# Kernel optimization log

Hardware: AMD Instinct MI355X
Metric: run time of the kernel (lower is better)

The kernel has to match this reference:

```python
import jax, jax.numpy as jnp
import numpy as np

KH, KW = 3, 3
STRIDE, PAD, DIL = 1, 1, 1
DG = 1  # deformable groups


def setup_inputs() -> dict:
    key = jax.random.key(0)
    k1, k2, k3, k4 = jax.random.split(key, 4)
    B, C, H, W, O = 4, 64, 128, 128, 64
    x = jax.random.normal(k1, (B, C, H, W), jnp.float32)
    weight = jax.random.normal(k2, (O, C, KH, KW), jnp.float32) * 0.05
    bias = jnp.zeros((O,), jnp.float32)
    # offset/mask conv params (zero-init in original; small random here so
    # the bilinear sampling path is actually exercised)
    om_weight = jax.random.normal(k3, (DG * 3 * KH * KW, C, KH, KW), jnp.float32) * 0.01
    om_bias = jax.random.normal(k4, (DG * 3 * KH * KW,), jnp.float32) * 0.01
    return {"x": x, "weight": weight, "bias": bias,
            "om_weight": om_weight, "om_bias": om_bias}


def _dcn(x, weight, bias, om_weight, om_bias):
    B, C, H, W = x.shape
    O = weight.shape[0]
    K = KH * KW
    Cg = C // DG

    # --- offset/mask conv (plain conv2d) ---
    om = jax.lax.conv_general_dilated(
        x, om_weight, (STRIDE, STRIDE), [(PAD, PAD), (PAD, PAD)],
        dimension_numbers=("NCHW", "OIHW", "NCHW"))
    om = om + om_bias[None, :, None, None]
    Ho, Wo = om.shape[2], om.shape[3]
    o1, o2, m = jnp.split(om, 3, axis=1)            # each (B, DG*K, Ho, Wo)
    off_y = o1.reshape(B, DG, K, Ho, Wo)
    off_x = o2.reshape(B, DG, K, Ho, Wo)
    mask = jax.nn.sigmoid(m).reshape(B, DG, K, Ho, Wo)

    # --- fractional sampling positions per kernel tap ---
    ky = jnp.repeat(jnp.arange(KH), KW).astype(jnp.float32)   # (K,)
    kx = jnp.tile(jnp.arange(KW), KH).astype(jnp.float32)
    base_y = (jnp.arange(Ho, dtype=jnp.float32) * STRIDE - PAD)
    base_x = (jnp.arange(Wo, dtype=jnp.float32) * STRIDE - PAD)
    py = off_y + base_y[None, None, None, :, None] + (ky * DIL)[None, None, :, None, None]
    px = off_x + base_x[None, None, None, None, :] + (kx * DIL)[None, None, :, None, None]

    y0 = jnp.floor(py)
    x0 = jnp.floor(px)
    ly = py - y0
    lx = px - x0
    y0i = y0.astype(jnp.int32)
    x0i = x0.astype(jnp.int32)

    xg = x.reshape(B, DG, Cg, H * W)
    # gather spatial samples per (batch, group), broadcast over channels
    gather = jax.vmap(jax.vmap(lambda feat, idx: jnp.take(feat, idx, axis=-1)))

    def corner(yc, xc, w):
        valid = (yc >= 0) & (yc < H) & (xc >= 0) & (xc < W)
        idx = jnp.clip(yc, 0, H - 1) * W + jnp.clip(xc, 0, W - 1)  # (B,DG,K,Ho,Wo)
        v = gather(xg, idx.reshape(B, DG, -1)).reshape(B, DG, Cg, K, Ho, Wo)
        w = jnp.where(valid, w, 0.0)
        return v * w[:, :, None]  # zero-padded bilinear corner

    val = (corner(y0i,     x0i,     (1 - ly) * (1 - lx))
         + corner(y0i,     x0i + 1, (1 - ly) * lx)
         + corner(y0i + 1, x0i,     ly * (1 - lx))
         + corner(y0i + 1, x0i + 1, ly * lx))
    val = val * mask[:, :, None]                    # (B,DG,Cg,K,Ho,Wo)

    w4 = weight.reshape(O, DG, Cg, K)
    out = jnp.einsum("ogck,bgckhw->bohw", w4, val) + bias[None, :, None, None]
    return out


def reference(x, weight, bias, om_weight, om_bias):
    return _dcn(x, weight, bias, om_weight, om_bias)
```

## Files before the change

kernel.cpp:

```cpp
#include <hip/hip_runtime.h>
#include <hip/hip_fp16.h>
#include <math.h>

#define BB 4
#define CC 64
#define HH 128
#define WW 128
#define OO 64
#define HWW (HH * WW)

typedef _Float16 f16x8 __attribute__((ext_vector_type(8)));
typedef float f32x4 __attribute__((ext_vector_type(4)));

#define WHF_OFF  0
#define WLF_OFF  73728
#define WOMH_OFF 147456
#define WOML_OFF 184320

__device__ inline __half2 u2h(unsigned u) {
    union { unsigned u; __half2 h; } c; c.u = u; return c.h;
}
__device__ inline unsigned h2u(__half2 h) {
    union { __half2 h; unsigned u; } c; c.h = h; return c.u;
}

__global__ void prep_kernel(const float* __restrict__ weight,
                            const float* __restrict__ om_weight,
                            unsigned short* __restrict__ whf,
                            unsigned short* __restrict__ wlf,
                            unsigned short* __restrict__ womh,
                            unsigned short* __restrict__ woml)
{
    int d = blockIdx.x * 256 + threadIdx.x;
    if (d < 18 * 4 * 64 * 8) {
        int j  = d & 7;
        int l  = (d >> 3) & 63;
        int wv = (d >> 9) & 3;
        int ch = d >> 11;
        int o  = wv * 16 + (l & 15);
        int kk = (l >> 4) * 8 + j;
        int c  = (ch / 9) * 32 + kk;
        int tap = ch % 9;
        float w = weight[(o * CC + c) * 9 + tap];
        __half h = __float2half_rn(w);
        __half lo = __float2half_rn(w - __half2float(h));
        whf[d] = __half_as_ushort(h);
        wlf[d] = __half_as_ushort(lo);
    }
    int d2 = d - 18 * 4 * 64 * 8;
    if (d2 >= 0 && d2 < 18 * 2 * 64 * 8) {
        int j  = d2 & 7;
        int l  = (d2 >> 3) & 63;
        int og = (d2 >> 9) & 1;
        int ch = d2 >> 10;
        int o  = og * 16 + (l & 15);
        int kk = (l >> 4) * 8 + j;
        int c  = (ch / 9) * 32 + kk;
        int tap = ch % 9;
        float w = (o < 27) ? om_weight[(o * CC + c) * 9 + tap] : 0.f;
        __half h = __float2half_rn(w);
        __half lo = __float2half_rn(w - __half2float(h));
        womh[d2] = __half_as_ushort(h);
        woml[d2] = __half_as_ushort(lo);
    }
}

__global__ void __launch_bounds__(256, 4)
fused_kernel(const float* __restrict__ x,
             const unsigned short* __restrict__ whf,
             const unsigned short* __restrict__ wlf,
             const unsigned short* __restrict__ womh,
             const unsigned short* __restrict__ woml,
             const float* __restrict__ bias,
             const float* __restrict__ om_bias,
             float* __restrict__ out)
{
    __shared__ __align__(16) uint4 Xw[8 * 180];
    __shared__ __align__(16) uint4 vex[2][32][9];
    __shared__ __align__(16) uint4 swth4[288];
    __shared__ int sidx[288];

    int t    = threadIdx.x;
    int lane = t & 63;
    int wv   = t >> 6;

    int bid = blockIdx.x;
    int b   = bid >> 9;
    int r   = bid & 511;
    int ho  = r >> 2;
    int w0  = (r & 3) << 5;

    {
        const float* xb = x + (size_t)b * CC * HWW;
#pragma unroll 1
        for (int i = t; i < 8 * 180; i += 256) {
            int cg  = i / 180;
            int pos = i - cg * 180;
            int rr  = pos / 36;
            int cc2 = pos - rr * 36;
            int gy = ho - 2 + rr, gx = w0 - 2 + cc2;
            bool ok = (gy >= 0) & (gy < HH) & (gx >= 0) & (gx < WW);
            int gi = ok ? gy * WW + gx : 0;
            const float* xc = xb + (size_t)cg * 8 * HWW + gi;
            float v0 = xc[0],       v1 = xc[HWW],     v2 = xc[2 * HWW], v3 = xc[3 * HWW];
            float v4 = xc[4 * HWW], v5 = xc[5 * HWW], v6 = xc[6 * HWW], v7 = xc[7 * HWW];
            if (!ok) { v0=0.f; v1=0.f; v2=0.f; v3=0.f; v4=0.f; v5=0.f; v6=0.f; v7=0.f; }
            uint4 p;
            p.x = h2u(__floats2half2_rn(v0, v1));
            p.y = h2u(__floats2half2_rn(v2, v3));
            p.z = h2u(__floats2half2_rn(v4, v5));
            p.w = h2u(__floats2half2_rn(v6, v7));
            Xw[cg * 180 + pos] = p;
        }
    }
    __syncthreads();

    f32x4 accom = (f32x4){0.f, 0.f, 0.f, 0.f};
    {
        int og = wv & 1;
        int s  = wv >> 1;
        int pix_s = s * 16 + (lane & 15);
        int oct   = lane >> 4;
#pragma unroll 1
        for (int ch = 0; ch < 18; ch++) {
            int half = ch / 9;
            int tap  = ch - half * 9;
            int ky = tap / 3, kx = tap - ky * 3;
            int pos = (ky + 1) * 36 + pix_s + kx + 1;
            uint4 pw = Xw[(half * 4 + oct) * 180 + pos];
            union { f16x8 v; uint4 u; } B; B.u = pw;
            const f16x8 ah = *(const f16x8*)&womh[((size_t)(ch * 2 + og) * 64 + lane) * 8];
            const f16x8 al = *(const f16x8*)&woml[((size_t)(ch * 2 + og) * 64 + lane) * 8];
            accom = __builtin_amdgcn_mfma_f32_16x16x32_f16(ah, B.v, accom, 0, 0, 0);
            accom = __builtin_amdgcn_mfma_f32_16x16x32_f16(al, B.v, accom, 0, 0, 0);
        }
    }

    float* omL = (float*)&vex[0][0][0];
    {
        int og = wv & 1, s = wv >> 1;
#pragma unroll
        for (int rg = 0; rg < 4; rg++) {
            int m = og * 16 + (lane >> 4) * 4 + rg;
            if (m < 27) {
                int pp = s * 16 + (lane & 15);
                float v = accom[rg] + om_bias[m];
                if (m >= 18) v = 1.f / (1.f + expf(-v));
                omL[m * 32 + pp] = v;
            }
        }
    }
    __syncthreads();

#pragma unroll 1
    for (int it = t; it < 288; it += 256) {
        int k  = it >> 5;
        int pp = it & 31;
        float oy = omL[k * 32 + pp];
        float ox = omL[(9 + k) * 32 + pp];
        float mm = omL[(18 + k) * 32 + pp];
        int ky = k / 3, kx = k - ky * 3;
        float py = oy + (float)(ho + ky - 1);
        float px = ox + (float)(w0 + pp + kx - 1);
        float fy = floorf(py), fx = floorf(px);
        float ly = py - fy, lx = px - fx;
        int y0 = (int)fy, x0 = (int)fx;
        bool vy0 = (y0 >= 0) & (y0 < HH);
        bool vy1 = (y0 + 1 >= 0) & (y0 + 1 < HH);
        bool vx0 = (x0 >= 0) & (x0 < WW);
        bool vx1 = (x0 + 1 >= 0) & (x0 + 1 < WW);
        float w00 = (vy0 & vx0) ? (1.f - ly) * (1.f - lx) * mm : 0.f;
        float w01 = (vy0 & vx1) ? (1.f - ly) * lx * mm : 0.f;
        float w10 = (vy1 & vx0) ? ly * (1.f - lx) * mm : 0.f;
        float w11 = (vy1 & vx1) ? ly * lx * mm : 0.f;
        uint4 wp;
        wp.x = h2u(__float2half2_rn(w00));
        wp.y = h2u(__float2half2_rn(w01));
        wp.z = h2u(__float2half2_rn(w10));
        wp.w = h2u(__float2half2_rn(w11));
        swth4[it] = wp;
        bool inw = (y0 >= ho - 2) & (y0 <= ho + 1) & (x0 >= w0 - 2) & (x0 <= w0 + 32);
        int y0c = min(max(y0, -8), 135);
        int x0c = min(max(x0, -8), 135);
        sidx[it] = ((y0c + 16) << 16) | ((x0c + 16) & 0xFFFF)
                 | (inw ? 0 : (int)0x80000000);
    }
    __syncthreads();

    f32x4 acc[2];
    acc[0] = (f32x4){0.f, 0.f, 0.f, 0.f};
    acc[1] = (f32x4){0.f, 0.f, 0.f, 0.f};

    {
        int pix = t & 31;
        int cg  = t >> 5;
#pragma unroll 1
        for (int tap = 0; tap < 9; tap++) {
            int buf  = tap & 1;
            int item = tap * 32 + pix;
            uint4 wp = swth4[item];
            int sv = sidx[item];
            int y0 = ((sv >> 16) & 0x7FFF) - 16;
            int x0 = (sv & 0xFFFF) - 16;
            const f16x8 ah0 = *(const f16x8*)&whf[((size_t)(tap * 4 + wv) * 64 + lane) * 8];
            const f16x8 al0 = *(const f16x8*)&wlf[((size_t)(tap * 4 + wv) * 64 + lane) * 8];
            const f16x8 ah1 = *(const f16x8*)&whf[((size_t)((9 + tap) * 4 + wv) * 64 + lane) * 8];
            const f16x8 al1 = *(const f16x8*)&wlf[((size_t)((9 + tap) * 4 + wv) * 64 + lane) * 8];

            uint4 payload;
            if (sv >= 0) {
                int o00 = (y0 - ho + 2) * 36 + (x0 - w0 + 2);
                const uint4* Xrow = &Xw[cg * 180];
                uint4 c00 = Xrow[o00];
                uint4 c01 = Xrow[o00 + 1];
                uint4 c10 = Xrow[o00 + 36];
                uint4 c11 = Xrow[o00 + 37];
                __half2 w00 = u2h(wp.x), w01 = u2h(wp.y);
                __half2 w10 = u2h(wp.z), w11 = u2h(wp.w);
                __half2 vA = __hmul2(w00, u2h(c00.x));
                vA = __hfma2(w01, u2h(c01.x), vA);
                vA = __hfma2(w10, u2h(c10.x), vA);
                vA = __hfma2(w11, u2h(c11.x), vA);
                __half2 vB = __hmul2(w00, u2h(c00.y));
                vB = __hfma2(w01, u2h(c01.y), vB);
                vB = __hfma2(w10, u2h(c10.y), vB);
                vB = __hfma2(w11, u2h(c11.y), vB);
                __half2 vC = __hmul2(w00, u2h(c00.z));
                vC = __hfma2(w01, u2h(c01.z), vC);
                vC = __hfma2(w10, u2h(c10.z), vC);
                vC = __hfma2(w11, u2h(c11.z), vC);
                __half2 vD = __hmul2(w00, u2h(c00.w));
                vD = __hfma2(w01, u2h(c01.w), vD);
                vD = __hfma2(w10, u2h(c10.w), vD);
                vD = __hfma2(w11, u2h(c11.w), vD);
                payload.x = h2u(vA); payload.y = h2u(vB);
                payload.z = h2u(vC); payload.w = h2u(vD);
            } else {
                const float* xg = x + ((size_t)(b * CC + cg * 8)) * HWW;
                float w00f = __low2float(u2h(wp.x)), w01f = __low2float(u2h(wp.y));
                float w10f = __low2float(u2h(wp.z)), w11f = __low2float(u2h(wp.w));
                int cy0 = min(max(y0, 0), HH - 1), cy1 = min(max(y0 + 1, 0), HH - 1);
                int cx0 = min(max(x0, 0), WW - 1), cx1 = min(max(x0 + 1, 0), WW - 1);
                int i00 = cy0 * WW + cx0, i01 = cy0 * WW + cx1;
                int i10 = cy1 * WW + cx0, i11 = cy1 * WW + cx1;
                float vv[8];
#pragma unroll
                for (int j = 0; j < 8; j++) {
                    const float* xc = xg + (size_t)j * HWW;
                    vv[j] = w00f * xc[i00] + w01f * xc[i01]
                          + w10f * xc[i10] + w11f * xc[i11];
                }
                payload.x = h2u(__floats2half2_rn(vv[0], vv[1]));
                payload.y = h2u(__floats2half2_rn(vv[2], vv[3]));
                payload.z = h2u(__floats2half2_rn(vv[4], vv[5]));
                payload.w = h2u(__floats2half2_rn(vv[6], vv[7]));
            }
            vex[buf][pix][cg] = payload;
            __syncthreads();
#pragma unroll
            for (int s2 = 0; s2 < 2; s2++) {
                union { f16x8 v; uint4 u; } B0, B1;
                B0.u = vex[buf][s2 * 16 + (lane & 15)][lane >> 4];
                B1.u = vex[buf][s2 * 16 + (lane & 15)][4 + (lane >> 4)];
                acc[s2] = __builtin_amdgcn_mfma_f32_16x16x32_f16(ah0, B0.v, acc[s2], 0, 0, 0);
                acc[s2] = __builtin_amdgcn_mfma_f32_16x16x32_f16(al0, B0.v, acc[s2], 0, 0, 0);
                acc[s2] = __builtin_amdgcn_mfma_f32_16x16x32_f16(ah1, B1.v, acc[s2], 0, 0, 0);
                acc[s2] = __builtin_amdgcn_mfma_f32_16x16x32_f16(al1, B1.v, acc[s2], 0, 0, 0);
            }
        }
    }

    int prow = ho * WW + w0;
#pragma unroll
    for (int s = 0; s < 2; s++) {
#pragma unroll
        for (int rg = 0; rg < 4; rg++) {
            int o  = wv * 16 + (lane >> 4) * 4 + rg;
            int pp = s * 16 + (lane & 15);
            out[((size_t)(b * OO + o)) * HWW + prow + pp] = acc[s][rg] + bias[o];
        }
    }
}

extern "C" void kernel_launch(void* const* d_in, const int* in_sizes, int n_in,
                              void* d_out, int out_size, void* d_ws, size_t ws_size,
                              hipStream_t stream)
{
    (void)in_sizes; (void)n_in; (void)out_size; (void)ws_size;
    const float* x      = (const float*)d_in[0];
    const float* weight = (const float*)d_in[1];
    const float* bias   = (const float*)d_in[2];
    const float* om_w   = (const float*)d_in[3];
    const float* om_b   = (const float*)d_in[4];
    float* out = (float*)d_out;
    char*  ws  = (char*)d_ws;

    unsigned short* whf  = (unsigned short*)(ws + WHF_OFF);
    unsigned short* wlf  = (unsigned short*)(ws + WLF_OFF);
    unsigned short* womh = (unsigned short*)(ws + WOMH_OFF);
    unsigned short* woml = (unsigned short*)(ws + WOML_OFF);

    int prep_n = 18 * 4 * 64 * 8 + 18 * 2 * 64 * 8;
    prep_kernel<<<(prep_n + 255) / 256, 256, 0, stream>>>(weight, om_w, whf, wlf, womh, woml);

    int nblk = BB * HH * (WW / 32);
    fused_kernel<<<nblk, 256, 0, stream>>>(x, whf, wlf, womh, woml, bias, om_b, out);
}
```

Baseline: 119.8 us.

## Drop split-fp16 weight correction and remap waves to pixels, removing per-tap barrier

```diff
diff --git a/kernel.cpp b/kernel.cpp
--- a/kernel.cpp
+++ b/kernel.cpp
@@ -13,9 +13,7 @@
 typedef float f32x4 __attribute__((ext_vector_type(4)));
 
 #define WHF_OFF  0
-#define WLF_OFF  73728
-#define WOMH_OFF 147456
-#define WOML_OFF 184320
+#define WOMH_OFF 73728
 
 __device__ inline __half2 u2h(unsigned u) {
     union { unsigned u; __half2 h; } c; c.u = u; return c.h;
@@ -27,25 +25,20 @@
 __global__ void prep_kernel(const float* __restrict__ weight,
                             const float* __restrict__ om_weight,
                             unsigned short* __restrict__ whf,
-                            unsigned short* __restrict__ wlf,
-                            unsigned short* __restrict__ womh,
-                            unsigned short* __restrict__ woml)
+                            unsigned short* __restrict__ womh)
 {
     int d = blockIdx.x * 256 + threadIdx.x;
     if (d < 18 * 4 * 64 * 8) {
         int j  = d & 7;
         int l  = (d >> 3) & 63;
-        int wv = (d >> 9) & 3;
+        int og = (d >> 9) & 3;
         int ch = d >> 11;
-        int o  = wv * 16 + (l & 15);
+        int o  = og * 16 + (l & 15);
         int kk = (l >> 4) * 8 + j;
         int c  = (ch / 9) * 32 + kk;
         int tap = ch % 9;
         float w = weight[(o * CC + c) * 9 + tap];
-        __half h = __float2half_rn(w);
-        __half lo = __float2half_rn(w - __half2float(h));
-        whf[d] = __half_as_ushort(h);
-        wlf[d] = __half_as_ushort(lo);
+        whf[d] = __half_as_ushort(__float2half_rn(w));
     }
     int d2 = d - 18 * 4 * 64 * 8;
     if (d2 >= 0 && d2 < 18 * 2 * 64 * 8) {
@@ -58,27 +51,22 @@
         int c  = (ch / 9) * 32 + kk;
         int tap = ch % 9;
         float w = (o < 27) ? om_weight[(o * CC + c) * 9 + tap] : 0.f;
-        __half h = __float2half_rn(w);
-        __half lo = __float2half_rn(w - __half2float(h));
-        womh[d2] = __half_as_ushort(h);
-        woml[d2] = __half_as_ushort(lo);
-    }
-}
-
-__global__ void __launch_bounds__(256, 4)
+        womh[d2] = __half_as_ushort(__float2half_rn(w));
+    }
+}
+
+__global__ void __launch_bounds__(128, 4)
 fused_kernel(const float* __restrict__ x,
              const unsigned short* __restrict__ whf,
-             const unsigned short* __restrict__ wlf,
              const unsigned short* __restrict__ womh,
-             const unsigned short* __restrict__ woml,
              const float* __restrict__ bias,
              const float* __restrict__ om_bias,
              float* __restrict__ out)
 {
     __shared__ __align__(16) uint4 Xw[8 * 180];
-    __shared__ __align__(16) uint4 vex[2][32][9];
     __shared__ __align__(16) uint4 swth4[288];
-    __shared__ int sidx[288];
+    __shared__ int   sidx[288];
+    __shared__ float omL[27 * 32];
 
     int t    = threadIdx.x;
     int lane = t & 63;
@@ -90,10 +78,14 @@
     int ho  = r >> 2;
     int w0  = (r & 3) << 5;
 
+    int pixl = lane & 15;
+    int pix  = wv * 16 + pixl;
+    int oct  = lane >> 4;
+
     {
         const float* xb = x + (size_t)b * CC * HWW;
 #pragma unroll 1
-        for (int i = t; i < 8 * 180; i += 256) {
+        for (int i = t; i < 8 * 180; i += 128) {
             int cg  = i / 180;
             int pos = i - cg * 180;
             int rr  = pos / 36;
@@ -115,45 +107,43 @@
     }
     __syncthreads();
 
-    f32x4 accom = (f32x4){0.f, 0.f, 0.f, 0.f};
+    f32x4 accom[2];
+    accom[0] = (f32x4){0.f, 0.f, 0.f, 0.f};
+    accom[1] = (f32x4){0.f, 0.f, 0.f, 0.f};
     {
-        int og = wv & 1;
-        int s  = wv >> 1;
-        int pix_s = s * 16 + (lane & 15);
-        int oct   = lane >> 4;
 #pragma unroll 1
         for (int ch = 0; ch < 18; ch++) {
             int half = ch / 9;
             int tap  = ch - half * 9;
             int ky = tap / 3, kx = tap - ky * 3;
-            int pos = (ky + 1) * 36 + pix_s + kx + 1;
-            uint4 pw = Xw[(half * 4 + oct) * 180 + pos];
-            union { f16x8 v; uint4 u; } B; B.u = pw;
-            const f16x8 ah = *(const f16x8*)&womh[((size_t)(ch * 2 + og) * 64 + lane) * 8];
-            const f16x8 al = *(const f16x8*)&woml[((size_t)(ch * 2 + og) * 64 + lane) * 8];
-            accom = __builtin_amdgcn_mfma_f32_16x16x32_f16(ah, B.v, accom, 0, 0, 0);
-            accom = __builtin_amdgcn_mfma_f32_16x16x32_f16(al, B.v, accom, 0, 0, 0);
-        }
-    }
-
-    float* omL = (float*)&vex[0][0][0];
+            int pos = (ky + 1) * 36 + pix + kx + 1;
+            union { f16x8 v; uint4 u; } B;
+            B.u = Xw[(half * 4 + oct) * 180 + pos];
+            const f16x8 a0 = *(const f16x8*)&womh[((size_t)(ch * 2 + 0) * 64 + lane) * 8];
+            const f16x8 a1 = *(const f16x8*)&womh[((size_t)(ch * 2 + 1) * 64 + lane) * 8];
+            accom[0] = __builtin_amdgcn_mfma_f32_16x16x32_f16(a0, B.v, accom[0], 0, 0, 0);
+            accom[1] = __builtin_amdgcn_mfma_f32_16x16x32_f16(a1, B.v, accom[1], 0, 0, 0);
+        }
+    }
+
     {
-        int og = wv & 1, s = wv >> 1;
-#pragma unroll
-        for (int rg = 0; rg < 4; rg++) {
-            int m = og * 16 + (lane >> 4) * 4 + rg;
-            if (m < 27) {
-                int pp = s * 16 + (lane & 15);
-                float v = accom[rg] + om_bias[m];
-                if (m >= 18) v = 1.f / (1.f + expf(-v));
-                omL[m * 32 + pp] = v;
+#pragma unroll
+        for (int og = 0; og < 2; og++) {
+#pragma unroll
+            for (int rg = 0; rg < 4; rg++) {
+                int m = og * 16 + (lane >> 4) * 4 + rg;
+                if (m < 27) {
+                    float v = accom[og][rg] + om_bias[m];
+                    if (m >= 18) v = 1.f / (1.f + expf(-v));
+                    omL[m * 32 + pix] = v;
+                }
             }
         }
     }
     __syncthreads();
 
 #pragma unroll 1
-    for (int it = t; it < 288; it += 256) {
+    for (int it = t; it < 288; it += 128) {
         int k  = it >> 5;
         int pp = it & 31;
         float oy = omL[k * 32 + pp];
@@ -187,36 +177,36 @@
     }
     __syncthreads();
 
-    f32x4 acc[2];
-    acc[0] = (f32x4){0.f, 0.f, 0.f, 0.f};
-    acc[1] = (f32x4){0.f, 0.f, 0.f, 0.f};
+    f32x4 acc[4];
+#pragma unroll
+    for (int og = 0; og < 4; og++) acc[og] = (f32x4){0.f, 0.f, 0.f, 0.f};
 
     {
-        int pix = t & 31;
-        int cg  = t >> 5;
+        int oct1 = 4 + oct;
 #pragma unroll 1
         for (int tap = 0; tap < 9; tap++) {
-            int buf  = tap & 1;
             int item = tap * 32 + pix;
             uint4 wp = swth4[item];
             int sv = sidx[item];
             int y0 = ((sv >> 16) & 0x7FFF) - 16;
             int x0 = (sv & 0xFFFF) - 16;
-            const f16x8 ah0 = *(const f16x8*)&whf[((size_t)(tap * 4 + wv) * 64 + lane) * 8];
-            const f16x8 al0 = *(const f16x8*)&wlf[((size_t)(tap * 4 + wv) * 64 + lane) * 8];
-            const f16x8 ah1 = *(const f16x8*)&whf[((size_t)((9 + tap) * 4 + wv) * 64 + lane) * 8];
-            const f16x8 al1 = *(const f16x8*)&wlf[((size_t)((9 + tap) * 4 + wv) * 64 + lane) * 8];
-
-            uint4 payload;
+            const f16x8 a00 = *(const f16x8*)&whf[((size_t)(tap * 4 + 0) * 64 + lane) * 8];
+            const f16x8 a01 = *(const f16x8*)&whf[((size_t)(tap * 4 + 1) * 64 + lane) * 8];
+            const f16x8 a02 = *(const f16x8*)&whf[((size_t)(tap * 4 + 2) * 64 + lane) * 8];
+            const f16x8 a03 = *(const f16x8*)&whf[((size_t)(tap * 4 + 3) * 64 + lane) * 8];
+            const f16x8 a10 = *(const f16x8*)&whf[((size_t)((9 + tap) * 4 + 0) * 64 + lane) * 8];
+            const f16x8 a11 = *(const f16x8*)&whf[((size_t)((9 + tap) * 4 + 1) * 64 + lane) * 8];
+            const f16x8 a12 = *(const f16x8*)&whf[((size_t)((9 + tap) * 4 + 2) * 64 + lane) * 8];
+            const f16x8 a13 = *(const f16x8*)&whf[((size_t)((9 + tap) * 4 + 3) * 64 + lane) * 8];
+
+            union { f16x8 v; uint4 u; } B0, B1;
             if (sv >= 0) {
                 int o00 = (y0 - ho + 2) * 36 + (x0 - w0 + 2);
-                const uint4* Xrow = &Xw[cg * 180];
-                uint4 c00 = Xrow[o00];
-                uint4 c01 = Xrow[o00 + 1];
-                uint4 c10 = Xrow[o00 + 36];
-                uint4 c11 = Xrow[o00 + 37];
                 __half2 w00 = u2h(wp.x), w01 = u2h(wp.y);
                 __half2 w10 = u2h(wp.z), w11 = u2h(wp.w);
+                const uint4* X0 = &Xw[oct * 180];
+                uint4 c00 = X0[o00], c01 = X0[o00 + 1];
+                uint4 c10 = X0[o00 + 36], c11 = X0[o00 + 37];
                 __half2 vA = __hmul2(w00, u2h(c00.x));
                 vA = __hfma2(w01, u2h(c01.x), vA);
                 vA = __hfma2(w10, u2h(c10.x), vA);
@@ -233,51 +223,73 @@
                 vD = __hfma2(w01, u2h(c01.w), vD);
                 vD = __hfma2(w10, u2h(c10.w), vD);
                 vD = __hfma2(w11, u2h(c11.w), vD);
-                payload.x = h2u(vA); payload.y = h2u(vB);
-                payload.z = h2u(vC); payload.w = h2u(vD);
+                B0.u.x = h2u(vA); B0.u.y = h2u(vB); B0.u.z = h2u(vC); B0.u.w = h2u(vD);
+                const uint4* X1 = &Xw[oct1 * 180];
+                uint4 d00 = X1[o00], d01 = X1[o00 + 1];
+                uint4 d10 = X1[o00 + 36], d11 = X1[o00 + 37];
+                __half2 uA = __hmul2(w00, u2h(d00.x));
+                uA = __hfma2(w01, u2h(d01.x), uA);
+                uA = __hfma2(w10, u2h(d10.x), uA);
+                uA = __hfma2(w11, u2h(d11.x), uA);
+                __half2 uB = __hmul2(w00, u2h(d00.y));
+                uB = __hfma2(w01, u2h(d01.y), uB);
+                uB = __hfma2(w10, u2h(d10.y), uB);
+                uB = __hfma2(w11, u2h(d11.y), uB);
+                __half2 uC = __hmul2(w00, u2h(d00.z));
+                uC = __hfma2(w01, u2h(d01.z), uC);
+                uC = __hfma2(w10, u2h(d10.z), uC);
+                uC = __hfma2(w11, u2h(d11.z), uC);
+                __half2 uD = __hmul2(w00, u2h(d00.w));
+                uD = __hfma2(w01, u2h(d01.w), uD);
+                uD = __hfma2(w10, u2h(d10.w), uD);
+                uD = __hfma2(w11, u2h(d11.w), uD);
+                B1.u.x = h2u(uA); B1.u.y = h2u(uB); B1.u.z = h2u(uC); B1.u.w = h2u(uD);
             } else {
-                const float* xg = x + ((size_t)(b * CC + cg * 8)) * HWW;
                 float w00f = __low2float(u2h(wp.x)), w01f = __low2float(u2h(wp.y));
                 float w10f = __low2float(u2h(wp.z)), w11f = __low2float(u2h(wp.w));
                 int cy0 = min(max(y0, 0), HH - 1), cy1 = min(max(y0 + 1, 0), HH - 1);
                 int cx0 = min(max(x0, 0), WW - 1), cx1 = min(max(x0 + 1, 0), WW - 1);
                 int i00 = cy0 * WW + cx0, i01 = cy0 * WW + cx1;
                 int i10 = cy1 * WW + cx0, i11 = cy1 * WW + cx1;
-                float vv[8];
+                float vv[8], uu[8];
+                const float* xg0 = x + ((size_t)(b * CC + oct * 8)) * HWW;
+                const float* xg1 = x + ((size_t)(b * CC + oct1 * 8)) * HWW;
 #pragma unroll
                 for (int j = 0; j < 8; j++) {
-                    const float* xc = xg + (size_t)j * HWW;
+                    const float* xc = xg0 + (size_t)j * HWW;
                     vv[j] = w00f * xc[i00] + w01f * xc[i01]
                           + w10f * xc[i10] + w11f * xc[i11];
+                    const float* xd = xg1 + (size_t)j * HWW;
+                    uu[j] = w00f * xd[i00] + w01f * xd[i01]
+                          + w10f * xd[i10] + w11f * xd[i11];
                 }
-                payload.x = h2u(__floats2half2_rn(vv[0], vv[1]));
-                payload.y = h2u(__floats2half2_rn(vv[2], vv[3]));
-                payload.z = h2u(__floats2half2_rn(vv[4], vv[5]));
-                payload.w = h2u(__floats2half2_rn(vv[6], vv[7]));
+                B0.u.x = h2u(__floats2half2_rn(vv[0], vv[1]));
+                B0.u.y = h2u(__floats2half2_rn(vv[2], vv[3]));
+                B0.u.z = h2u(__floats2half2_rn(vv[4], vv[5]));
+                B0.u.w = h2u(__floats2half2_rn(vv[6], vv[7]));
+                B1.u.x = h2u(__floats2half2_rn(uu[0], uu[1]));
+                B1.u.y = h2u(__floats2half2_rn(uu[2], uu[3]));
+                B1.u.z = h2u(__floats2half2_rn(uu[4], uu[5]));
+                B1.u.w = h2u(__floats2half2_rn(uu[6], uu[7]));
             }
-            vex[buf][pix][cg] = payload;
-            __syncthreads();
-#pragma unroll
-            for (int s2 = 0; s2 < 2; s2++) {
-                union { f16x8 v; uint4 u; } B0, B1;
-                B0.u = vex[buf][s2 * 16 + (lane & 15)][lane >> 4];
-                B1.u = vex[buf][s2 * 16 + (lane & 15)][4 + (lane >> 4)];
-                acc[s2] = __builtin_amdgcn_mfma_f32_16x16x32_f16(ah0, B0.v, acc[s2], 0, 0, 0);
-                acc[s2] = __builtin_amdgcn_mfma_f32_16x16x32_f16(al0, B0.v, acc[s2], 0, 0, 0);
-                acc[s2] = __builtin_amdgcn_mfma_f32_16x16x32_f16(ah1, B1.v, acc[s2], 0, 0, 0);
-                acc[s2] = __builtin_amdgcn_mfma_f32_16x16x32_f16(al1, B1.v, acc[s2], 0, 0, 0);
-            }
+            acc[0] = __builtin_amdgcn_mfma_f32_16x16x32_f16(a00, B0.v, acc[0], 0, 0, 0);
+            acc[1] = __builtin_amdgcn_mfma_f32_16x16x32_f16(a01, B0.v, acc[1], 0, 0, 0);
+            acc[2] = __builtin_amdgcn_mfma_f32_16x16x32_f16(a02, B0.v, acc[2], 0, 0, 0);
+            acc[3] = __builtin_amdgcn_mfma_f32_16x16x32_f16(a03, B0.v, acc[3], 0, 0, 0);
+            acc[0] = __builtin_amdgcn_mfma_f32_16x16x32_f16(a10, B1.v, acc[0], 0, 0, 0);
+            acc[1] = __builtin_amdgcn_mfma_f32_16x16x32_f16(a11, B1.v, acc[1], 0, 0, 0);
+            acc[2] = __builtin_amdgcn_mfma_f32_16x16x32_f16(a12, B1.v, acc[2], 0, 0, 0);
+            acc[3] = __builtin_amdgcn_mfma_f32_16x16x32_f16(a13, B1.v, acc[3], 0, 0, 0);
         }
     }
 
     int prow = ho * WW + w0;
 #pragma unroll
-    for (int s = 0; s < 2; s++) {
+    for (int og = 0; og < 4; og++) {
 #pragma unroll
         for (int rg = 0; rg < 4; rg++) {
-            int o  = wv * 16 + (lane >> 4) * 4 + rg;
-            int pp = s * 16 + (lane & 15);
-            out[((size_t)(b * OO + o)) * HWW + prow + pp] = acc[s][rg] + bias[o];
+            int o = og * 16 + (lane >> 4) * 4 + rg;
+            out[((size_t)(b * OO + o)) * HWW + prow + pix] = acc[og][rg] + bias[o];
         }
     }
 }
@@ -296,13 +308,11 @@
     char*  ws  = (char*)d_ws;
 
     unsigned short* whf  = (unsigned short*)(ws + WHF_OFF);
-    unsigned short* wlf  = (unsigned short*)(ws + WLF_OFF);
     unsigned short* womh = (unsigned short*)(ws + WOMH_OFF);
-    unsigned short* woml = (unsigned short*)(ws + WOML_OFF);
 
     int prep_n = 18 * 4 * 64 * 8 + 18 * 2 * 64 * 8;
-    prep_kernel<<<(prep_n + 255) / 256, 256, 0, stream>>>(weight, om_w, whf, wlf, womh, woml);
+    prep_kernel<<<(prep_n + 255) / 256, 256, 0, stream>>>(weight, om_w, whf, womh);
 
     int nblk = BB * HH * (WW / 32);
-    fused_kernel<<<nblk, 256, 0, stream>>>(x, whf, wlf, womh, woml, bias, om_b, out);
-}
+    fused_kernel<<<nblk, 128, 0, stream>>>(x, whf, womh, bias, om_b, out);
+}
```

Measured after the change: 122.4 us. 1.02x slower.

## Drop fp16 hi/lo weight split and remap waves to output-channel pairs

Applied to the files above, without the earlier changes.

```diff
diff --git a/kernel.cpp b/kernel.cpp
--- a/kernel.cpp
+++ b/kernel.cpp
@@ -13,9 +13,7 @@
 typedef float f32x4 __attribute__((ext_vector_type(4)));
 
 #define WHF_OFF  0
-#define WLF_OFF  73728
-#define WOMH_OFF 147456
-#define WOML_OFF 184320
+#define WOMH_OFF 73728
 
 __device__ inline __half2 u2h(unsigned u) {
     union { unsigned u; __half2 h; } c; c.u = u; return c.h;
@@ -27,25 +25,20 @@
 __global__ void prep_kernel(const float* __restrict__ weight,
                             const float* __restrict__ om_weight,
                             unsigned short* __restrict__ whf,
-                            unsigned short* __restrict__ wlf,
-                            unsigned short* __restrict__ womh,
-                            unsigned short* __restrict__ woml)
+                            unsigned short* __restrict__ womh)
 {
     int d = blockIdx.x * 256 + threadIdx.x;
     if (d < 18 * 4 * 64 * 8) {
         int j  = d & 7;
         int l  = (d >> 3) & 63;
-        int wv = (d >> 9) & 3;
+        int og = (d >> 9) & 3;
         int ch = d >> 11;
-        int o  = wv * 16 + (l & 15);
+        int o  = og * 16 + (l & 15);
         int kk = (l >> 4) * 8 + j;
         int c  = (ch / 9) * 32 + kk;
         int tap = ch % 9;
         float w = weight[(o * CC + c) * 9 + tap];
-        __half h = __float2half_rn(w);
-        __half lo = __float2half_rn(w - __half2float(h));
-        whf[d] = __half_as_ushort(h);
-        wlf[d] = __half_as_ushort(lo);
+        whf[d] = __half_as_ushort(__float2half_rn(w));
     }
     int d2 = d - 18 * 4 * 64 * 8;
     if (d2 >= 0 && d2 < 18 * 2 * 64 * 8) {
@@ -58,19 +51,14 @@
         int c  = (ch / 9) * 32 + kk;
         int tap = ch % 9;
         float w = (o < 27) ? om_weight[(o * CC + c) * 9 + tap] : 0.f;
-        __half h = __float2half_rn(w);
-        __half lo = __float2half_rn(w - __half2float(h));
-        womh[d2] = __half_as_ushort(h);
-        woml[d2] = __half_as_ushort(lo);
+        womh[d2] = __half_as_ushort(__float2half_rn(w));
     }
 }
 
 __global__ void __launch_bounds__(256, 4)
 fused_kernel(const float* __restrict__ x,
              const unsigned short* __restrict__ whf,
-             const unsigned short* __restrict__ wlf,
              const unsigned short* __restrict__ womh,
-             const unsigned short* __restrict__ woml,
              const float* __restrict__ bias,
              const float* __restrict__ om_bias,
              float* __restrict__ out)
@@ -127,12 +115,10 @@
             int tap  = ch - half * 9;
             int ky = tap / 3, kx = tap - ky * 3;
             int pos = (ky + 1) * 36 + pix_s + kx + 1;
-            uint4 pw = Xw[(half * 4 + oct) * 180 + pos];
-            union { f16x8 v; uint4 u; } B; B.u = pw;
-            const f16x8 ah = *(const f16x8*)&womh[((size_t)(ch * 2 + og) * 64 + lane) * 8];
-            const f16x8 al = *(const f16x8*)&woml[((size_t)(ch * 2 + og) * 64 + lane) * 8];
-            accom = __builtin_amdgcn_mfma_f32_16x16x32_f16(ah, B.v, accom, 0, 0, 0);
-            accom = __builtin_amdgcn_mfma_f32_16x16x32_f16(al, B.v, accom, 0, 0, 0);
+            union { f16x8 v; uint4 u; } B;
+            B.u = Xw[(half * 4 + oct) * 180 + pos];
+            const f16x8 a0 = *(const f16x8*)&womh[((size_t)(ch * 2 + og) * 64 + lane) * 8];
+            accom = __builtin_amdgcn_mfma_f32_16x16x32_f16(a0, B.v, accom, 0, 0, 0);
         }
     }
 
@@ -187,6 +173,11 @@
     }
     __syncthreads();
 
+    int og2  = wv >> 1;
+    int s2   = wv & 1;
+    int pixl = lane & 15;
+    int oct  = lane >> 4;
+
     f32x4 acc[2];
     acc[0] = (f32x4){0.f, 0.f, 0.f, 0.f};
     acc[1] = (f32x4){0.f, 0.f, 0.f, 0.f};
@@ -202,10 +193,10 @@
             int sv = sidx[item];
             int y0 = ((sv >> 16) & 0x7FFF) - 16;
             int x0 = (sv & 0xFFFF) - 16;
-            const f16x8 ah0 = *(const f16x8*)&whf[((size_t)(tap * 4 + wv) * 64 + lane) * 8];
-            const f16x8 al0 = *(const f16x8*)&wlf[((size_t)(tap * 4 + wv) * 64 + lane) * 8];
-            const f16x8 ah1 = *(const f16x8*)&whf[((size_t)((9 + tap) * 4 + wv) * 64 + lane) * 8];
-            const f16x8 al1 = *(const f16x8*)&wlf[((size_t)((9 + tap) * 4 + wv) * 64 + lane) * 8];
+            const f16x8 a00 = *(const f16x8*)&whf[((size_t)(tap * 4 + og2 * 2 + 0) * 64 + lane) * 8];
+            const f16x8 a01 = *(const f16x8*)&whf[((size_t)(tap * 4 + og2 * 2 + 1) * 64 + lane) * 8];
+            const f16x8 a10 = *(const f16x8*)&whf[((size_t)((9 + tap) * 4 + og2 * 2 + 0) * 64 + lane) * 8];
+            const f16x8 a11 = *(const f16x8*)&whf[((size_t)((9 + tap) * 4 + og2 * 2 + 1) * 64 + lane) * 8];
 
             uint4 payload;
             if (sv >= 0) {
@@ -257,27 +248,26 @@
             }
             vex[buf][pix][cg] = payload;
             __syncthreads();
-#pragma unroll
-            for (int s2 = 0; s2 < 2; s2++) {
+            {
                 union { f16x8 v; uint4 u; } B0, B1;
-                B0.u = vex[buf][s2 * 16 + (lane & 15)][lane >> 4];
-                B1.u = vex[buf][s2 * 16 + (lane & 15)][4 + (lane >> 4)];
-                acc[s2] = __builtin_amdgcn_mfma_f32_16x16x32_f16(ah0, B0.v, acc[s2], 0, 0, 0);
-                acc[s2] = __builtin_amdgcn_mfma_f32_16x16x32_f16(al0, B0.v, acc[s2], 0, 0, 0);
-                acc[s2] = __builtin_amdgcn_mfma_f32_16x16x32_f16(ah1, B1.v, acc[s2], 0, 0, 0);
-                acc[s2] = __builtin_amdgcn_mfma_f32_16x16x32_f16(al1, B1.v, acc[s2], 0, 0, 0);
+                B0.u = vex[buf][s2 * 16 + pixl][oct];
+                B1.u = vex[buf][s2 * 16 + pixl][4 + oct];
+                acc[0] = __builtin_amdgcn_mfma_f32_16x16x32_f16(a00, B0.v, acc[0], 0, 0, 0);
+                acc[1] = __builtin_amdgcn_mfma_f32_16x16x32_f16(a01, B0.v, acc[1], 0, 0, 0);
+                acc[0] = __builtin_amdgcn_mfma_f32_16x16x32_f16(a10, B1.v, acc[0], 0, 0, 0);
+                acc[1] = __builtin_amdgcn_mfma_f32_16x16x32_f16(a11, B1.v, acc[1], 0, 0, 0);
             }
         }
     }
 
     int prow = ho * WW + w0;
 #pragma unroll
-    for (int s = 0; s < 2; s++) {
+    for (int a = 0; a < 2; a++) {
 #pragma unroll
         for (int rg = 0; rg < 4; rg++) {
-            int o  = wv * 16 + (lane >> 4) * 4 + rg;
-            int pp = s * 16 + (lane & 15);
-            out[((size_t)(b * OO + o)) * HWW + prow + pp] = acc[s][rg] + bias[o];
+            int o  = (og2 * 2 + a) * 16 + (lane >> 4) * 4 + rg;
+            int pp = s2 * 16 + pixl;
+            out[((size_t)(b * OO + o)) * HWW + prow + pp] = acc[a][rg] + bias[o];
         }
     }
 }
@@ -296,13 +286,11 @@
     char*  ws  = (char*)d_ws;
 
     unsigned short* whf  = (unsigned short*)(ws + WHF_OFF);
-    unsigned short* wlf  = (unsigned short*)(ws + WLF_OFF);
     unsigned short* womh = (unsigned short*)(ws + WOMH_OFF);
-    unsigned short* woml = (unsigned short*)(ws + WOML_OFF);
 
     int prep_n = 18 * 4 * 64 * 8 + 18 * 2 * 64 * 8;
-    prep_kernel<<<(prep_n + 255) / 256, 256, 0, stream>>>(weight, om_w, whf, wlf, womh, woml);
+    prep_kernel<<<(prep_n + 255) / 256, 256, 0, stream>>>(weight, om_w, whf, womh);
 
     int nblk = BB * HH * (WW / 32);
-    fused_kernel<<<nblk, 256, 0, stream>>>(x, whf, wlf, womh, woml, bias, om_b, out);
-}
+    fused_kernel<<<nblk, 256, 0, stream>>>(x, whf, womh, bias, om_b, out);
+}
```

Measured after the change: 109.8 us. -8.3%, faster.
